# Kernel optimization log

Measured on AMD Instinct MI355X. Metric: run time of the kernel, lower is better.

The kernel has to match this reference:

```python
import jax, jax.numpy as jnp
from jax import lax
import numpy as np

B, S, PRE = 64, 12, 12
N04, N07, N08 = 307, 883, 170
IN_DIM, HID, ENC = 128, 256, 256


def setup_inputs() -> dict:
    key = jax.random.key(0)
    ks = iter(jax.random.split(key, 64))
    nrm = lambda shape, s=1.0: jax.random.normal(next(ks), shape, jnp.float32) * s
    uni = lambda shape: jax.random.uniform(next(ks), shape, jnp.float32)
    d = {
        "vec_pems04": nrm((N04, IN_DIM)),
        "vec_pems07": nrm((N07, IN_DIM)),
        "vec_pems08": nrm((N08, IN_DIM)),
        "feat": nrm((B, S, N04)),
        "adj_pems04": uni((N04, N04)),
        "adj_pems07": uni((N07, N07)),
        "adj_pems08": uni((N08, N08)),
    }
    for p in ("ex4", "ex7", "ex8"):
        d[p + "_W1"] = nrm((IN_DIM, HID), 0.05)
        d[p + "_b1"] = jnp.zeros((HID,), jnp.float32)
        d[p + "_W2"] = nrm((HID, ENC), 0.05)
        d[p + "_b2"] = jnp.zeros((ENC,), jnp.float32)
        d[p + "_g"] = jnp.ones((ENC,), jnp.float32)
        d[p + "_bt"] = jnp.zeros((ENC,), jnp.float32)
        d[p + "_eps"] = jnp.ones((1,), jnp.float32)
    d["gru_W1"] = nrm((HID + 1, 2 * HID), 0.05)
    d["gru_b1"] = jnp.ones((2 * HID,), jnp.float32)  # VGRULinear bias=1.0
    d["gru_W2"] = nrm((HID + 1, HID), 0.05)
    d["gru_b2"] = jnp.zeros((HID,), jnp.float32)
    d["feat_W"] = nrm((ENC, ENC), 0.05)
    d["feat_b"] = jnp.zeros((1,), jnp.float32)
    d["lin_W"] = nrm((HID + ENC, HID), 0.05)
    d["lin_b"] = jnp.zeros((HID,), jnp.float32)
    d["out_W"] = nrm((HID, PRE), 0.05)
    d["out_b"] = jnp.zeros((PRE,), jnp.float32)
    d["eval_flag"] = 0
    return d


def _extract(vec, adj, W1, b1, W2, b2, g, bt, eps1):
    # Extractor_N2V with etype='gin', BatchNorm1d in training mode (batch stats)
    h = vec @ W1 + b1
    pooled = adj @ h
    deg = adj @ jnp.ones((adj.shape[0], 1), adj.dtype)
    h = pooled / deg + eps1 * h
    mu = jnp.mean(h, axis=0)
    var = jnp.mean(jnp.square(h - mu), axis=0)  # biased var, as torch BN
    h = (h - mu) * lax.rsqrt(var + 1e-5) * g + bt
    return h @ W2 + b2


def _predict(feat, node_feat, gru_W1, gru_b1, gru_W2, gru_b2, feat_W, feat_b, lin_W, lin_b):
    Bb, Ss, N = feat.shape
    H = gru_W2.shape[1]
    E = node_feat.shape[-1]
    # feat @ weights + bias is timestep-invariant -> hoist out of the scan (same math)
    fp = jnp.broadcast_to(node_feat[None], (Bb, N, E)).reshape(Bb * N, E) @ feat_W + feat_b

    def vl(x, hs, W, b):
        # VGRULinear: concat scalar input with per-node hidden, flatten per node
        cat = jnp.concatenate([x[..., None], hs.reshape(Bb, N, H)], axis=2).reshape(Bb * N, H + 1)
        return (cat @ W + b).reshape(Bb, -1)

    def step(h, x):
        gates = jax.nn.sigmoid(vl(x, h, gru_W1, gru_b1))  # (B, N*2H)
        r, u = jnp.split(gates, 2, axis=1)                # chunk on flat dim, as in source
        c = jnp.tanh(vl(x, r * h, gru_W2, gru_b2))
        nh = u * h + (1.0 - u) * c
        nh = jnp.concatenate([nh.reshape(Bb * N, H), fp], axis=1) @ lin_W + lin_b
        nh = nh.reshape(Bb, N * H)
        return nh, None

    h0 = jnp.zeros((Bb, N * H), feat.dtype)
    hT, _ = lax.scan(step, h0, jnp.swapaxes(feat, 0, 1))  # scan over seq_len
    return hT.reshape(Bb * N, H)  # last output


def reference(vec_pems04, vec_pems07, vec_pems08, feat, adj_pems04, adj_pems07, adj_pems08,
              ex4_W1, ex4_b1, ex4_W2, ex4_b2, ex4_g, ex4_bt, ex4_eps,
              ex7_W1, ex7_b1, ex7_W2, ex7_b2, ex7_g, ex7_bt, ex7_eps,
              ex8_W1, ex8_b1, ex8_W2, ex8_b2, ex8_g, ex8_bt, ex8_eps,
              gru_W1, gru_b1, gru_W2, gru_b2, feat_W, feat_b, lin_W, lin_b,
              out_W, out_b, eval_flag):
    # dataset='4' != ft_dataset='8', eval=False branch
    f4 = _extract(vec_pems04, adj_pems04, ex4_W1, ex4_b1, ex4_W2, ex4_b2, ex4_g, ex4_bt, ex4_eps)
    f7 = _extract(vec_pems07, adj_pems07, ex7_W1, ex7_b1, ex7_W2, ex7_b2, ex7_g, ex7_bt, ex7_eps)
    f8 = _extract(vec_pems08, adj_pems08, ex8_W1, ex8_b1, ex8_W2, ex8_b2, ex8_g, ex8_bt, ex8_eps)
    last = _predict(feat, f4, gru_W1, gru_b1, gru_W2, gru_b2, feat_W, feat_b, lin_W, lin_b)
    pred = (last @ out_W + out_b).reshape(feat.shape[0], adj_pems04.shape[0], -1)
    return pred, f4, f7, f8
```

## Files before the change

### kernel.cpp

```cpp
#include <hip/hip_runtime.h>
#include <hip/hip_bf16.h>
#include <math.h>

using bf16 = __hip_bfloat16;
using short8  = __attribute__((ext_vector_type(8))) short;
using float4v = __attribute__((ext_vector_type(4))) float;

#define B_   64
#define S_   12
#define N04  307
#define N07  883
#define N08  170
#define BN   (B_ * N04)
#define HID  256
#define ENC  256
#define PRE  12
#define UOFF (N04 * HID)

constexpr int c_Mi[3]   = {N04, N07, N08};
constexpr int c_Kp[3]   = {320, 896, 192};
constexpr int c_Moff[3] = {0, N04, N04 + N07};
constexpr int c_Aoff[3] = {0, N04 * 320, N04 * 320 + N07 * 896};
constexpr int c_Cb[3]   = {0, 320, 320 + 896};
#define MTOT  (N04 + N07 + N08)
#define H0T_LD 1408

#define NT 38
constexpr int g_sz[NT] = {
    39296, 113024, 21760, 235776, 94249, 779689, 28900,
    32768, 256, 65536, 256, 256, 256, 1,
    32768, 256, 65536, 256, 256, 256, 1,
    32768, 256, 65536, 256, 256, 256, 1,
    131584, 512, 65792, 256, 65536, 1, 131072, 256, 3072, 12
};
struct Tables { int off[NT + 1]; int blk[NT + 1]; };
constexpr Tables mk_tables() {
    Tables t{};
    t.off[0] = 0; t.blk[0] = 0;
    for (int i = 0; i < NT; ++i) {
        t.off[i + 1] = t.off[i] + g_sz[i];
        t.blk[i + 1] = t.blk[i] + (g_sz[i] + 1023) / 1024;
    }
    return t;
}
constexpr Tables g_tbl = mk_tables();

static __device__ __forceinline__ float fsigmoid(float t) {
    return __builtin_amdgcn_rcpf(1.f + __expf(-t));
}
static __device__ __forceinline__ float ftanh(float t) {
    return 1.f - 2.f * __builtin_amdgcn_rcpf(__expf(2.f * t) + 1.f);
}

static __device__ __forceinline__ void bsplit(int m, int& b, int& nn) {
    b  = (int)(((unsigned long long)(unsigned)m * 27980243ull) >> 33);
    nn = m - b * N04;
}

__global__ void sniff_kernel(const unsigned short* raw, int* flag)
{
    __shared__ int sh[256];
    int t = threadIdx.x, cnt = 0;
    for (int i = t; i < 2048; i += 256) {
        unsigned int w = ((unsigned int)raw[i]) << 16;
        float a = fabsf(__uint_as_float(w));
        if (a > 1e-3f && a < 100.f) cnt++;
    }
    sh[t] = cnt; __syncthreads();
    for (int off = 128; off > 0; off >>= 1) {
        if (t < off) sh[t] += sh[t + off];
        __syncthreads();
    }
    if (t == 0) *flag = (sh[0] > 1536) ? 1 : 0;
}

struct Ptrs { const void* p[NT]; };

__global__ __launch_bounds__(256) void convert_all(Ptrs a, float* arena, const int* flag)
{
    const int bf = *flag;
    int b = blockIdx.x;
    int t = 0;
    while (b >= g_tbl.blk[t + 1]) ++t;
    const int base = (b - g_tbl.blk[t]) * 1024;
    const int n = g_sz[t];
    const void* src = a.p[t];
    float* dst = arena + g_tbl.off[t];
#pragma unroll
    for (int k = 0; k < 4; ++k) {
        int j = base + k * 256 + threadIdx.x;
        if (j < n)
            dst[j] = bf ? __bfloat162float(((const bf16*)src)[j]) : ((const float*)src)[j];
    }
}

__global__ __launch_bounds__(256) void prep_weights(const float* w1, const float* w2, const float* wl,
                                                    bf16* WgP, bf16* WcP, bf16* WlP)
{
    int id = blockIdx.x * 256 + threadIdx.x;
    if (id < 131072) {
        int tile = id >> 9, within = id & 511;
        int lane = within >> 3, e = within & 7;
        int n = (tile >> 3) * 16 + (lane & 15);
        int k = (tile & 7) * 32 + (lane >> 4) * 8 + e;
        WgP[id] = __float2bfloat16(w1[(size_t)(1 + k) * 512 + n]);
    } else if (id < 196608) {
        int r = id - 131072;
        int tile = r >> 9, within = r & 511;
        int lane = within >> 3, e = within & 7;
        int n = (tile >> 3) * 16 + (lane & 15);
        int k = (tile & 7) * 32 + (lane >> 4) * 8 + e;
        WcP[r] = __float2bfloat16(w2[(size_t)(1 + k) * 256 + n]);
    } else if (id < 262144) {
        int r = id - 196608;
        int tile = r >> 9, within = r & 511;
        int lane = within >> 3, e = within & 7;
        int n = (tile >> 3) * 16 + (lane & 15);
        int k = (tile & 7) * 32 + (lane >> 4) * 8 + e;
        WlP[r] = __float2bfloat16(wl[(size_t)k * 256 + n]);
    }
}

__global__ __launch_bounds__(256) void prep_adjB(const float* a4, const float* a7, const float* a8, bf16* adjB)
{
    int z = blockIdx.z;
    int Mi = c_Mi[z], Kp = c_Kp[z];
    int m = blockIdx.x;
    if (m >= Mi) return;
    const float* src = (z == 0) ? a4 : (z == 1) ? a7 : a8;
    bf16* dst = adjB + c_Aoff[z] + (size_t)m * Kp;
    for (int c = threadIdx.x; c < Kp; c += 256)
        dst[c] = (c < Mi) ? __float2bfloat16(src[(size_t)m * Mi + c]) : __float2bfloat16(0.f);
}

__global__ __launch_bounds__(256) void prep_transposes(
    const float* v4, const float* v7, const float* v8,
    const float* w1a, const float* w1b, const float* w1c,
    const float* w2a, const float* w2b, const float* w2c,
    const float* featW, const float* linW, const float* outW,
    bf16* vecB, bf16* W1T, bf16* W2T, bf16* featWT, bf16* linW2T, bf16* outWP)
{
    int id = blockIdx.x * 256 + threadIdx.x;
    if (id < 174080) {
        int r = id >> 7, c = id & 127;
        float v = (r < N04) ? v4[(size_t)r * 128 + c]
                : (r < N04 + N07) ? v7[(size_t)(r - N04) * 128 + c]
                : v8[(size_t)(r - N04 - N07) * 128 + c];
        vecB[id] = __float2bfloat16(v);
    } else if (id < 174080 + 98304) {
        int r = id - 174080; int z = r >> 15; int rem = r & 32767;
        int n = rem >> 7, k = rem & 127;
        const float* w = (z == 0) ? w1a : (z == 1) ? w1b : w1c;
        W1T[r] = __float2bfloat16(w[(size_t)k * 256 + n]);
    } else if (id < 272384 + 196608) {
        int r = id - 272384; int z = r >> 16; int rem = r & 65535;
        int n = rem >> 8, k = rem & 255;
        const float* w = (z == 0) ? w2a : (z == 1) ? w2b : w2c;
        W2T[r] = __float2bfloat16(w[(size_t)k * 256 + n]);
    } else if (id < 468992 + 65536) {
        int r = id - 468992; int n = r >> 8, k = r & 255;
        featWT[r] = __float2bfloat16(featW[(size_t)k * 256 + n]);
    } else if (id < 534528 + 65536) {
        int r = id - 534528; int n = r >> 8, k = r & 255;
        linW2T[r] = __float2bfloat16(linW[(size_t)(256 + k) * 256 + n]);
    } else if (id < 600064 + 16384) {
        int r = id - 600064;
        int tile = r >> 9, within = r & 511;
        int lane = within >> 3, e = within & 7;
        int p = (tile >> 3) * 16 + (lane & 15);
        int k = (tile & 7) * 32 + (lane >> 4) * 8 + e;
        outWP[r] = __float2bfloat16((p < PRE) ? outW[(size_t)k * PRE + p] : 0.f);
    }
}
#define PREP_T_TOT (600064 + 16384)

struct GemmZ {
    const unsigned short* A[3];
    const unsigned short* BT[3];
    int M[3]; int K[3]; int lda[3]; int ldb[3];
};

template <typename EP>
__global__ __launch_bounds__(256) void gemm_mfma64(GemmZ p, int Nv, EP ep)
{
    const int z = blockIdx.z;
    const int gx = gridDim.x, gy = gridDim.y;
    const int nwg = gx * gy;
    const int flat = blockIdx.y * gx + blockIdx.x;
    const int xcd = flat & 7, lin = flat >> 3;
    const int q = nwg >> 3, r = nwg & 7;
    const int wg = (xcd < r ? xcd * (q + 1) : r * (q + 1) + (xcd - r) * q) + lin;
    const int bx = wg / gy;
    const int by = wg - bx * gy;

    const int M = p.M[z], K = p.K[z], lda = p.lda[z], ldb = p.ldb[z];
    const int m0 = bx * 64;
    const int n0 = by * 64;
    if (m0 >= M) return;
    __shared__ __align__(16) unsigned short As[64 * 72];
    __shared__ __align__(16) unsigned short Bs[64 * 72];
    const int t = threadIdx.x;
    const int srow  = t >> 2;
    const int skoff = (t & 3) * 16;
    const int lane = t & 63;
    const int w  = t >> 6;
    const int wm = (w & 1) * 32;
    const int wn = (w >> 1) * 32;
    const int l15 = lane & 15;
    const int l4  = lane >> 4;

    float4v acc[2][2];
#pragma unroll
    for (int i = 0; i < 2; ++i)
#pragma unroll
        for (int j = 0; j < 2; ++j) acc[i][j] = (float4v)(0.f);

    const int gm = m0 + srow;
    const bool avalid = (gm < M);
    const unsigned short* aptr = p.A[z]  + (size_t)gm * lda + skoff;
    const unsigned short* bptr = p.BT[z] + (size_t)(n0 + srow) * ldb + skoff;
    unsigned short* asw = &As[srow * 72 + skoff];
    unsigned short* bsw = &Bs[srow * 72 + skoff];
    const uint4 z4 = {0, 0, 0, 0};

    for (int kt = 0; kt < K; kt += 64) {
        uint4 av0 = avalid ? *(const uint4*)(aptr + kt)     : z4;
        uint4 av1 = avalid ? *(const uint4*)(aptr + kt + 8) : z4;
        uint4 bv0 = *(const uint4*)(bptr + kt);
        uint4 bv1 = *(const uint4*)(bptr + kt + 8);
        __syncthreads();
        *(uint4*)(asw)     = av0;
        *(uint4*)(asw + 8) = av1;
        *(uint4*)(bsw)     = bv0;
        *(uint4*)(bsw + 8) = bv1;
        __syncthreads();
#pragma unroll
        for (int ks = 0; ks < 2; ++ks) {
            short8 af[2], bq[2];
#pragma unroll
            for (int mi = 0; mi < 2; ++mi)
                af[mi] = *(const short8*)&As[(wm + mi * 16 + l15) * 72 + ks * 32 + l4 * 8];
#pragma unroll
            for (int ni = 0; ni < 2; ++ni)
                bq[ni] = *(const short8*)&Bs[(wn + ni * 16 + l15) * 72 + ks * 32 + l4 * 8];
#pragma unroll
            for (int mi = 0; mi < 2; ++mi)
#pragma unroll
                for (int ni = 0; ni < 2; ++ni)
                    acc[mi][ni] = __builtin_amdgcn_mfma_f32_16x16x32_bf16(af[mi], bq[ni], acc[mi][ni], 0, 0, 0);
        }
    }
#pragma unroll
    for (int mi = 0; mi < 2; ++mi) {
#pragma unroll
        for (int r2 = 0; r2 < 4; ++r2) {
            int m = m0 + wm + mi * 16 + l4 * 4 + r2;
            if (m >= M) continue;
#pragma unroll
            for (int ni = 0; ni < 2; ++ni) {
                int n = n0 + wn + ni * 16 + l15;
                if (n < Nv) ep(z, m, n, acc[mi][ni][r2]);
            }
        }
    }
}

struct GemmB { const unsigned short* A; const unsigned short* Bp; int M; };

template <typename EP>
__global__ __launch_bounds__(256, 4) void gemm_bd(GemmB p, int Nv, EP ep)
{
    const int gx = gridDim.x, gy = gridDim.y;
    const int nwg = gx * gy;
    const int flat = blockIdx.y * gx + blockIdx.x;
    const int xcd = flat & 7, lin = flat >> 3;
    const int q = nwg >> 3, r = nwg & 7;
    const int wg = (xcd < r ? xcd * (q + 1) : r * (q + 1) + (xcd - r) * q) + lin;
    const int bx = wg / gy;
    const int by = wg - bx * gy;
    const int m0 = bx * 64;
    const int n0 = by * 64;

    __shared__ __align__(16) unsigned short As[64 * 72];
    const int t = threadIdx.x;
    const int srow  = t >> 2;
    const int skoff = (t & 3) * 16;
    const int lane = t & 63;
    const int w  = t >> 6;
    const int wm = (w & 1) * 32;
    const int wn = (w >> 1) * 32;
    const int l15 = lane & 15;
    const int l4  = lane >> 4;

    float4v acc[2][2];
#pragma unroll
    for (int i = 0; i < 2; ++i)
#pragma unroll
        for (int j = 0; j < 2; ++j) acc[i][j] = (float4v)(0.f);

    const unsigned short* aptr = p.A + (size_t)(m0 + srow) * 256 + skoff;
    unsigned short* asw = &As[srow * 72 + skoff];
    const unsigned short* bbase = p.Bp + (((size_t)((n0 + wn) >> 4) * 8) << 9) + (lane << 3);

#pragma unroll
    for (int kt = 0; kt < 4; ++kt) {
        uint4 av0 = *(const uint4*)(aptr + kt * 64);
        uint4 av1 = *(const uint4*)(aptr + kt * 64 + 8);
        __syncthreads();
        *(uint4*)(asw)     = av0;
        *(uint4*)(asw + 8) = av1;
        __syncthreads();
#pragma unroll
        for (int ks = 0; ks < 2; ++ks) {
            const int kc = kt * 2 + ks;
            short8 af[2], bq[2];
#pragma unroll
            for (int mi = 0; mi < 2; ++mi)
                af[mi] = *(const short8*)&As[(wm + mi * 16 + l15) * 72 + ks * 32 + l4 * 8];
            bq[0] = *(const short8*)(bbase + ((size_t)kc << 9));
            bq[1] = *(const short8*)(bbase + ((size_t)(kc + 8) << 9));
#pragma unroll
            for (int mi = 0; mi < 2; ++mi)
#pragma unroll
                for (int ni = 0; ni < 2; ++ni)
                    acc[mi][ni] = __builtin_amdgcn_mfma_f32_16x16x32_bf16(af[mi], bq[ni], acc[mi][ni], 0, 0, 0);
        }
    }
#pragma unroll
    for (int mi = 0; mi < 2; ++mi) {
#pragma unroll
        for (int r2 = 0; r2 < 4; ++r2) {
            const int m = m0 + wm + mi * 16 + l4 * 4 + r2;
#pragma unroll
            for (int ni = 0; ni < 2; ++ni) {
                const int n = n0 + wn + ni * 16 + l15;
                if (n < Nv) ep(0, m, n, acc[mi][ni][r2]);
            }
        }
    }
}

struct EPg1 {
    const float* b1[3]; float* h0F; bf16* h0T;
    __device__ void operator()(int z, int m, int n, float v) const {
        v += b1[z][n];
        int gr = c_Moff[z] + m;
        h0F[(size_t)gr * 256 + n] = v;
        h0T[(size_t)n * H0T_LD + c_Cb[z] + m] = __float2bfloat16(v);
    }
};
struct EPg2 {
    const float* deg; const float* h0F; float* h1F; const float* eps[3];
    __device__ void operator()(int z, int m, int n, float v) const {
        int gr = c_Moff[z] + m;
        h1F[(size_t)gr * 256 + n] = v / deg[gr] + eps[z][0] * h0F[(size_t)gr * 256 + n];
    }
};
struct EPg3 {
    const float* b2[3]; void* outbase; size_t ooff[3]; const int* flag; bf16* f4B;
    __device__ void operator()(int z, int m, int n, float v) const {
        v += b2[z][n];
        size_t i = ooff[z] + (size_t)m * 256 + n;
        if (*flag) ((bf16*)outbase)[i] = __float2bfloat16(v);
        else       ((float*)outbase)[i] = v;
        if (z == 0) f4B[(size_t)m * 256 + n] = __float2bfloat16(v);
    }
};
struct EPfp2a {
    const float* sb; bf16* fpreB;
    __device__ void operator()(int z, int m, int n, float v) const {
        fpreB[(size_t)m * 256 + n] = __float2bfloat16(v + sb[0]);
    }
};
struct EPfp2b {
    float* fp2;
    __device__ void operator()(int z, int m, int n, float v) const {
        fp2[(size_t)m * 256 + n] = v;
    }
};
struct EPpred {
    const float* ob; void* outbase; const int* flag;
    __device__ void operator()(int z, int m, int n, float v) const {
        v += ob[n];
        size_t i = (size_t)m * PRE + n;
        if (*flag) ((bf16*)outbase)[i] = __float2bfloat16(v);
        else       ((float*)outbase)[i] = v;
    }
};

struct EPgates3 {
    bf16* rh; bf16* ub; const bf16* hB;
    const float* b1; const float* w1r0; const float* feat; int s;
    __device__ void operator()(int z, int m, int n, float v) const {
        int b, nn; bsplit(m, b, nn);
        float x = feat[((size_t)b * S_ + s) * N04 + nn];
        float g = fsigmoid(v + b1[n] + x * w1r0[n]);
        int p = nn * 512 + n;
        int base = b * UOFF;
        if (p < UOFF) {
            int idx = base + p;
            rh[idx] = __float2bfloat16(g * __bfloat162float(hB[idx]));
        } else {
            ub[base + (p - UOFF)] = __float2bfloat16(g);
        }
    }
};
struct EPcand3 {
    bf16* uhc; const bf16* ub; const bf16* hB;
    const float* b2; const float* w2r0; const float* feat; int s;
    __device__ void operator()(int z, int m, int n, float v) const {
        int b, nn; bsplit(m, b, nn);
        float x = feat[((size_t)b * S_ + s) * N04 + nn];
        float c = ftanh(v + b2[n] + x * w2r0[n]);
        size_t idx = (size_t)m * 256 + n;
        float u = __bfloat162float(ub[idx]);
        float h = __bfloat162float(hB[idx]);
        uhc[idx] = __float2bfloat16(u * h + (1.f - u) * c);
    }
};
struct EPlin3 {
    bf16* hB; const float* lb; const float* fp2;
    __device__ void operator()(int z, int m, int n, float v) const {
        int b, nn; bsplit(m, b, nn);
        hB[(size_t)m * 256 + n] = __float2bfloat16(v + lb[n] + fp2[(size_t)nn * 256 + n]);
    }
};

__global__ __launch_bounds__(256) void init_step0(const float* feat,
                                                  const float* b1, const float* w1r0,
                                                  const float* b2, const float* w2r0,
                                                  bf16* uhc)
{
    int m = blockIdx.x, n = threadIdx.x;
    int b, nn; bsplit(m, b, nn);
    const float* fb = feat + (size_t)b * S_ * N04;
    float c = ftanh(b2[n] + fb[nn] * w2r0[n]);
    int p = UOFF + nn * 256 + n;
    int gn = p >> 9, gc = p & 511;
    float u = fsigmoid(b1[gc] + fb[gn] * w1r0[gc]);
    uhc[(size_t)m * 256 + n] = __float2bfloat16((1.f - u) * c);
}

__global__ void deg_all(const float* a4, const float* a7, const float* a8, float* deg)
{
    int z = blockIdx.z;
    int Mi = c_Mi[z];
    int row = blockIdx.x;
    if (row >= Mi) return;
    const float* adj = (z == 0) ? a4 : (z == 1) ? a7 : a8;
    float s = 0.f;
    for (int j = threadIdx.x; j < Mi; j += 64) s += adj[(size_t)row * Mi + j];
#pragma unroll
    for (int off = 32; off > 0; off >>= 1) s += __shfl_down(s, off, 64);
    if (threadIdx.x == 0) deg[c_Moff[z] + row] = s;
}

__global__ __launch_bounds__(256) void stats_all(const float* h1F, float* mu, float* rstd)
{
    int z = blockIdx.z;
    int Mi = c_Mi[z], moff = c_Moff[z];
    int j = blockIdx.x;
    int t = threadIdx.x;
    float s = 0.f, ss = 0.f;
    for (int i = t; i < Mi; i += 256) {
        float v = h1F[(size_t)(moff + i) * 256 + j];
        s += v; ss += v * v;
    }
    __shared__ float sh[256], sh2[256];
    sh[t] = s; sh2[t] = ss;
    __syncthreads();
    for (int off = 128; off > 0; off >>= 1) {
        if (t < off) { sh[t] += sh[t + off]; sh2[t] += sh2[t + off]; }
        __syncthreads();
    }
    if (t == 0) {
        float m = sh[0] / (float)Mi;
        float var = sh2[0] / (float)Mi - m * m;
        mu[z * 256 + j] = m;
        rstd[z * 256 + j] = rsqrtf(var + 1e-5f);
    }
}

__global__ __launch_bounds__(256) void norm_all(const float* h1F, const float* mu, const float* rstd,
                                                const float* ga, const float* gb, const float* gc,
                                                const float* ba, const float* bb, const float* bc,
                                                bf16* nh1B)
{
    int r = blockIdx.x;
    int n = threadIdx.x;
    int z = (r < N04) ? 0 : (r < N04 + N07) ? 1 : 2;
    const float* g  = (z == 0) ? ga : (z == 1) ? gb : gc;
    const float* bt = (z == 0) ? ba : (z == 1) ? bb : bc;
    float v = (h1F[(size_t)r * 256 + n] - mu[z * 256 + n]) * rstd[z * 256 + n] * g[n] + bt[n];
    nh1B[(size_t)r * 256 + n] = __float2bfloat16(v);
}

extern "C" void kernel_launch(void* const* d_in, const int* in_sizes, int n_in,
                              void* d_out, int out_size, void* d_ws, size_t ws_size,
                              hipStream_t stream)
{
    char* wp = (char*)d_ws;
    auto carve = [&](size_t bytes) -> void* {
        void* p = (void*)wp;
        wp += (bytes + 255) & ~(size_t)255;
        return p;
    };
    float* arena = (float*)carve((size_t)g_tbl.off[NT] * 4);
    int*   flag  = (int*)carve(256);
    bf16*  hb_a  = (bf16*)carve((size_t)BN * HID * 2);
    bf16*  hb_b  = (bf16*)carve((size_t)BN * HID * 2);
    bf16*  rh    = (bf16*)carve((size_t)BN * HID * 2);
    bf16*  uhc   = (bf16*)carve((size_t)BN * HID * 2);
    bf16*  ubufB = (bf16*)carve((size_t)BN * HID * 2);
    bf16*  WgP   = (bf16*)carve((size_t)512 * 256 * 2);
    bf16*  WcP   = (bf16*)carve((size_t)256 * 256 * 2);
    bf16*  WlP   = (bf16*)carve((size_t)256 * 256 * 2);
    bf16*  vecB  = (bf16*)carve((size_t)MTOT * 128 * 2);
    bf16*  adjB  = (bf16*)carve((size_t)(N04 * 320 + N07 * 896 + N08 * 192) * 2);
    bf16*  W1T   = (bf16*)carve((size_t)3 * 256 * 128 * 2);
    bf16*  W2T   = (bf16*)carve((size_t)3 * 256 * 256 * 2);
    bf16*  featWT= (bf16*)carve((size_t)256 * 256 * 2);
    bf16*  linW2T= (bf16*)carve((size_t)256 * 256 * 2);
    bf16*  outWP = (bf16*)carve((size_t)64 * 256 * 2);
    float* h0F   = (float*)carve((size_t)MTOT * 256 * 4);
    bf16*  h0T   = (bf16*)carve((size_t)256 * H0T_LD * 2);
    float* h1F   = (float*)carve((size_t)MTOT * 256 * 4);
    bf16*  nh1B  = (bf16*)carve((size_t)MTOT * 256 * 2);
    float* degb  = (float*)carve((size_t)MTOT * 4);
    float* mub   = (float*)carve(3 * 256 * 4);
    float* rstdb = (float*)carve(3 * 256 * 4);
    bf16*  f4B   = (bf16*)carve((size_t)N04 * 256 * 2);
    bf16*  fpreB = (bf16*)carve((size_t)N04 * 256 * 2);
    float* fp2   = (float*)carve((size_t)N04 * 256 * 4);

    sniff_kernel<<<1, 256, 0, stream>>>((const unsigned short*)d_in[0], flag);
    Ptrs ptrs;
    for (int i = 0; i < NT; ++i) ptrs.p[i] = d_in[i];
    convert_all<<<g_tbl.blk[NT], 256, 0, stream>>>(ptrs, arena, flag);

    auto A = [&](int i) -> const float* { return arena + g_tbl.off[i]; };

    prep_weights<<<1024, 256, 0, stream>>>(A(28), A(30), A(34), WgP, WcP, WlP);
    prep_adjB<<<dim3(N07, 1, 3), 256, 0, stream>>>(A(4), A(5), A(6), adjB);
    prep_transposes<<<(PREP_T_TOT + 255) / 256, 256, 0, stream>>>(
        A(0), A(1), A(2), A(7), A(14), A(21), A(9), A(16), A(23),
        A(32), A(34), A(36), vecB, W1T, W2T, featWT, linW2T, outWP);

    hipMemsetAsync(h0T, 0, (size_t)256 * H0T_LD * 2, stream);

    const size_t o_f4 = (size_t)B_ * N04 * PRE;
    const size_t o_f7 = o_f4 + (size_t)N04 * ENC;
    const size_t o_f8 = o_f7 + (size_t)N07 * ENC;

    deg_all<<<dim3(N07, 1, 3), 64, 0, stream>>>(A(4), A(5), A(6), degb);

    {
        GemmZ p;
        for (int z = 0; z < 3; ++z) {
            p.A[z] = (const unsigned short*)(vecB + (size_t)c_Moff[z] * 128);
            p.BT[z] = (const unsigned short*)(W1T + (size_t)z * 256 * 128);
            p.M[z] = c_Mi[z]; p.K[z] = 128; p.lda[z] = 128; p.ldb[z] = 128;
        }
        EPg1 ep{{A(8), A(15), A(22)}, h0F, h0T};
        gemm_mfma64<<<dim3(14, 4, 3), 256, 0, stream>>>(p, 256, ep);
    }
    {
        GemmZ p;
        for (int z = 0; z < 3; ++z) {
            p.A[z] = (const unsigned short*)(adjB + c_Aoff[z]);
            p.BT[z] = (const unsigned short*)(h0T + c_Cb[z]);
            p.M[z] = c_Mi[z]; p.K[z] = c_Kp[z]; p.lda[z] = c_Kp[z]; p.ldb[z] = H0T_LD;
        }
        EPg2 ep{degb, h0F, h1F, {A(13), A(20), A(27)}};
        gemm_mfma64<<<dim3(14, 4, 3), 256, 0, stream>>>(p, 256, ep);
    }
    stats_all<<<dim3(256, 1, 3), 256, 0, stream>>>(h1F, mub, rstdb);
    norm_all<<<MTOT, 256, 0, stream>>>(h1F, mub, rstdb, A(11), A(18), A(25), A(12), A(19), A(26), nh1B);
    {
        GemmZ p;
        for (int z = 0; z < 3; ++z) {
            p.A[z] = (const unsigned short*)(nh1B + (size_t)c_Moff[z] * 256);
            p.BT[z] = (const unsigned short*)(W2T + (size_t)z * 256 * 256);
            p.M[z] = c_Mi[z]; p.K[z] = 256; p.lda[z] = 256; p.ldb[z] = 256;
        }
        EPg3 ep{{A(10), A(17), A(24)}, d_out, {o_f4, o_f7, o_f8}, flag, f4B};
        gemm_mfma64<<<dim3(14, 4, 3), 256, 0, stream>>>(p, 256, ep);
    }
    {
        GemmZ p{};
        p.A[0] = (const unsigned short*)f4B; p.BT[0] = (const unsigned short*)featWT;
        p.M[0] = N04; p.K[0] = 256; p.lda[0] = 256; p.ldb[0] = 256;
        gemm_mfma64<<<dim3(5, 4, 1), 256, 0, stream>>>(p, 256, EPfp2a{A(33), fpreB});
        p.A[0] = (const unsigned short*)fpreB; p.BT[0] = (const unsigned short*)linW2T;
        gemm_mfma64<<<dim3(5, 4, 1), 256, 0, stream>>>(p, 256, EPfp2b{fp2});
    }

    const float* feat = A(3);
    bf16* hcB = hb_a;
    bf16* hnB = hb_b;
    for (int s = 0; s < S_; ++s) {
        if (s == 0) {
            init_step0<<<BN, 256, 0, stream>>>(feat, A(29), A(28), A(31), A(30), uhc);
        } else {
            GemmB pg{(const unsigned short*)hcB, (const unsigned short*)WgP, BN};
            gemm_bd<<<dim3(BN / 64, 8, 1), 256, 0, stream>>>(pg, 512,
                EPgates3{rh, ubufB, hcB, A(29), A(28), feat, s});
            GemmB pc{(const unsigned short*)rh, (const unsigned short*)WcP, BN};
            gemm_bd<<<dim3(BN / 64, 4, 1), 256, 0, stream>>>(pc, 256,
                EPcand3{uhc, ubufB, hcB, A(31), A(30), feat, s});
        }
        GemmB pl{(const unsigned short*)uhc, (const unsigned short*)WlP, BN};
        gemm_bd<<<dim3(BN / 64, 4, 1), 256, 0, stream>>>(pl, 256,
            EPlin3{hnB, A(35), fp2});
        bf16* tb = hcB; hcB = hnB; hnB = tb;
    }

    {
        GemmB pp{(const unsigned short*)hcB, (const unsigned short*)outWP, BN};
        gemm_bd<<<dim3(BN / 64, 1, 1), 256, 0, stream>>>(pp, PRE, EPpred{A(37), d_out, flag});
    }
}
```

Before: 743.8 us.

## Fuse GRU candidate and output-linear GEMMs into one kernel, fold degree into adj prep

Adds a gru_cl kernel that computes the candidate GEMM and its tanh/update epilogue, stages the resulting hidden state in shared memory, and immediately runs the output-linear GEMM on it. This removes the uhc global round trip and one launch per timestep, and folds the step-0 init into the same kernel. The degree row-sum is also computed inside prep_adjB, so the separate deg_all launch goes away. In exchange, each block now covers the full 256-wide N tile with 64 accumulators per thread and a large shared-memory footprint, which may lower occupancy.

Result: slower. 1.302 ms (+75.1%).

```diff
diff --git a/kernel.cpp b/kernel.cpp
--- a/kernel.cpp
+++ b/kernel.cpp
@@ -121,7 +121,8 @@
     }
 }
 
-__global__ __launch_bounds__(256) void prep_adjB(const float* a4, const float* a7, const float* a8, bf16* adjB)
+__global__ __launch_bounds__(256) void prep_adjB(const float* a4, const float* a7, const float* a8,
+                                                 bf16* adjB, float* deg)
 {
     int z = blockIdx.z;
     int Mi = c_Mi[z], Kp = c_Kp[z];
@@ -129,8 +130,19 @@
     if (m >= Mi) return;
     const float* src = (z == 0) ? a4 : (z == 1) ? a7 : a8;
     bf16* dst = adjB + c_Aoff[z] + (size_t)m * Kp;
-    for (int c = threadIdx.x; c < Kp; c += 256)
-        dst[c] = (c < Mi) ? __float2bfloat16(src[(size_t)m * Mi + c]) : __float2bfloat16(0.f);
+    float s = 0.f;
+    for (int c = threadIdx.x; c < Kp; c += 256) {
+        float v = (c < Mi) ? src[(size_t)m * Mi + c] : 0.f;
+        dst[c] = __float2bfloat16(v);
+        s += v;
+    }
+    __shared__ float sh[256];
+    sh[threadIdx.x] = s; __syncthreads();
+    for (int off = 128; off > 0; off >>= 1) {
+        if (threadIdx.x < off) sh[threadIdx.x] += sh[threadIdx.x + off];
+        __syncthreads();
+    }
+    if (threadIdx.x == 0) deg[c_Moff[z] + m] = sh[0];
 }
 
 __global__ __launch_bounds__(256) void prep_transposes(
@@ -340,6 +352,131 @@
     }
 }
 
+struct GruCL {
+    const unsigned short* rhA; const bf16* ub; const bf16* hB;
+    const unsigned short* WcP; const unsigned short* WlP;
+    const float* b2; const float* w2r0; const float* feat;
+    const float* lb; const float* fp2;
+    const float* b1; const float* w1r0;
+    bf16* hn; int s;
+};
+
+template <int STEP0>
+__global__ __launch_bounds__(256) void gru_cl(GruCL p)
+{
+    __shared__ __align__(16) unsigned short As[64 * 72];
+    __shared__ __align__(16) unsigned short U[64 * 264];
+    const int t = threadIdx.x;
+    const int lane = t & 63, w = t >> 6;
+    const int wm = (w & 1) * 32;
+    const int wn = (w >> 1) * 128;
+    const int l15 = lane & 15, l4 = lane >> 4;
+    const int m0 = blockIdx.x * 64;
+    const int srow = t >> 2, skoff = (t & 3) * 16;
+
+    if (STEP0) {
+        for (int j = t; j < 64 * 256; j += 256) {
+            int r_loc = j >> 8, n = j & 255;
+            int b, nn; bsplit(m0 + r_loc, b, nn);
+            const float* fb = p.feat + (size_t)b * S_ * N04;
+            float c = ftanh(p.b2[n] + fb[nn] * p.w2r0[n]);
+            int pf = UOFF + nn * 256 + n;
+            int gn = pf >> 9, gc = pf & 511;
+            float u = fsigmoid(p.b1[gc] + fb[gn] * p.w1r0[gc]);
+            ((bf16*)U)[r_loc * 264 + n] = __float2bfloat16((1.f - u) * c);
+        }
+    } else {
+        float4v acc[2][8];
+#pragma unroll
+        for (int i = 0; i < 2; ++i)
+#pragma unroll
+            for (int j = 0; j < 8; ++j) acc[i][j] = (float4v)(0.f);
+        const unsigned short* aptr = p.rhA + (size_t)(m0 + srow) * 256 + skoff;
+        unsigned short* asw = &As[srow * 72 + skoff];
+        const unsigned short* bbase = p.WcP + (((size_t)(wn >> 4) * 8) << 9) + (lane << 3);
+#pragma unroll
+        for (int kt = 0; kt < 4; ++kt) {
+            uint4 av0 = *(const uint4*)(aptr + kt * 64);
+            uint4 av1 = *(const uint4*)(aptr + kt * 64 + 8);
+            __syncthreads();
+            *(uint4*)(asw)     = av0;
+            *(uint4*)(asw + 8) = av1;
+            __syncthreads();
+#pragma unroll
+            for (int ks = 0; ks < 2; ++ks) {
+                const int kc = kt * 2 + ks;
+                short8 af[2];
+#pragma unroll
+                for (int mi = 0; mi < 2; ++mi)
+                    af[mi] = *(const short8*)&As[(wm + mi * 16 + l15) * 72 + ks * 32 + l4 * 8];
+#pragma unroll
+                for (int ni = 0; ni < 8; ++ni) {
+                    short8 bq = *(const short8*)(bbase + (((size_t)ni * 8 + kc) << 9));
+                    acc[0][ni] = __builtin_amdgcn_mfma_f32_16x16x32_bf16(af[0], bq, acc[0][ni], 0, 0, 0);
+                    acc[1][ni] = __builtin_amdgcn_mfma_f32_16x16x32_bf16(af[1], bq, acc[1][ni], 0, 0, 0);
+                }
+            }
+        }
+        float xr[2][4];
+#pragma unroll
+        for (int mi = 0; mi < 2; ++mi)
+#pragma unroll
+            for (int r2 = 0; r2 < 4; ++r2) {
+                int b, nn; bsplit(m0 + wm + mi * 16 + l4 * 4 + r2, b, nn);
+                xr[mi][r2] = p.feat[((size_t)b * S_ + p.s) * N04 + nn];
+            }
+#pragma unroll
+        for (int mi = 0; mi < 2; ++mi)
+#pragma unroll
+            for (int r2 = 0; r2 < 4; ++r2) {
+                const int r_loc = wm + mi * 16 + l4 * 4 + r2;
+                const size_t mrow = (size_t)(m0 + r_loc) * 256;
+#pragma unroll
+                for (int ni = 0; ni < 8; ++ni) {
+                    const int n = wn + ni * 16 + l15;
+                    float c = ftanh(acc[mi][ni][r2] + p.b2[n] + xr[mi][r2] * p.w2r0[n]);
+                    float u = __bfloat162float(p.ub[mrow + n]);
+                    float h = __bfloat162float(p.hB[mrow + n]);
+                    ((bf16*)U)[r_loc * 264 + n] = __float2bfloat16(u * h + (1.f - u) * c);
+                }
+            }
+    }
+    __syncthreads();
+
+    float4v acl[2][8];
+#pragma unroll
+    for (int i = 0; i < 2; ++i)
+#pragma unroll
+        for (int j = 0; j < 8; ++j) acl[i][j] = (float4v)(0.f);
+    const unsigned short* lbase = p.WlP + (((size_t)(wn >> 4) * 8) << 9) + (lane << 3);
+#pragma unroll
+    for (int kc = 0; kc < 8; ++kc) {
+        short8 af[2];
+#pragma unroll
+        for (int mi = 0; mi < 2; ++mi)
+            af[mi] = *(const short8*)&U[(wm + mi * 16 + l15) * 264 + kc * 32 + l4 * 8];
+#pragma unroll
+        for (int ni = 0; ni < 8; ++ni) {
+            short8 bq = *(const short8*)(lbase + (((size_t)ni * 8 + kc) << 9));
+            acl[0][ni] = __builtin_amdgcn_mfma_f32_16x16x32_bf16(af[0], bq, acl[0][ni], 0, 0, 0);
+            acl[1][ni] = __builtin_amdgcn_mfma_f32_16x16x32_bf16(af[1], bq, acl[1][ni], 0, 0, 0);
+        }
+    }
+#pragma unroll
+    for (int mi = 0; mi < 2; ++mi)
+#pragma unroll
+        for (int r2 = 0; r2 < 4; ++r2) {
+            const int m = m0 + wm + mi * 16 + l4 * 4 + r2;
+            int b, nn; bsplit(m, b, nn);
+#pragma unroll
+            for (int ni = 0; ni < 8; ++ni) {
+                const int n = wn + ni * 16 + l15;
+                p.hn[(size_t)m * 256 + n] =
+                    __float2bfloat16(acl[mi][ni][r2] + p.lb[n] + p.fp2[(size_t)nn * 256 + n]);
+            }
+        }
+}
+
 struct EPg1 {
     const float* b1[3]; float* h0F; bf16* h0T;
     __device__ void operator()(int z, int m, int n, float v) const {
@@ -405,55 +542,6 @@
         }
     }
 };
-struct EPcand3 {
-    bf16* uhc; const bf16* ub; const bf16* hB;
-    const float* b2; const float* w2r0; const float* feat; int s;
-    __device__ void operator()(int z, int m, int n, float v) const {
-        int b, nn; bsplit(m, b, nn);
-        float x = feat[((size_t)b * S_ + s) * N04 + nn];
-        float c = ftanh(v + b2[n] + x * w2r0[n]);
-        size_t idx = (size_t)m * 256 + n;
-        float u = __bfloat162float(ub[idx]);
-        float h = __bfloat162float(hB[idx]);
-        uhc[idx] = __float2bfloat16(u * h + (1.f - u) * c);
-    }
-};
-struct EPlin3 {
-    bf16* hB; const float* lb; const float* fp2;
-    __device__ void operator()(int z, int m, int n, float v) const {
-        int b, nn; bsplit(m, b, nn);
-        hB[(size_t)m * 256 + n] = __float2bfloat16(v + lb[n] + fp2[(size_t)nn * 256 + n]);
-    }
-};
-
-__global__ __launch_bounds__(256) void init_step0(const float* feat,
-                                                  const float* b1, const float* w1r0,
-                                                  const float* b2, const float* w2r0,
-                                                  bf16* uhc)
-{
-    int m = blockIdx.x, n = threadIdx.x;
-    int b, nn; bsplit(m, b, nn);
-    const float* fb = feat + (size_t)b * S_ * N04;
-    float c = ftanh(b2[n] + fb[nn] * w2r0[n]);
-    int p = UOFF + nn * 256 + n;
-    int gn = p >> 9, gc = p & 511;
-    float u = fsigmoid(b1[gc] + fb[gn] * w1r0[gc]);
-    uhc[(size_t)m * 256 + n] = __float2bfloat16((1.f - u) * c);
-}
-
-__global__ void deg_all(const float* a4, const float* a7, const float* a8, float* deg)
-{
-    int z = blockIdx.z;
-    int Mi = c_Mi[z];
-    int row = blockIdx.x;
-    if (row >= Mi) return;
-    const float* adj = (z == 0) ? a4 : (z == 1) ? a7 : a8;
-    float s = 0.f;
-    for (int j = threadIdx.x; j < Mi; j += 64) s += adj[(size_t)row * Mi + j];
-#pragma unroll
-    for (int off = 32; off > 0; off >>= 1) s += __shfl_down(s, off, 64);
-    if (threadIdx.x == 0) deg[c_Moff[z] + row] = s;
-}
 
 __global__ __launch_bounds__(256) void stats_all(const float* h1F, float* mu, float* rstd)
 {
@@ -510,7 +598,6 @@
     bf16*  hb_a  = (bf16*)carve((size_t)BN * HID * 2);
     bf16*  hb_b  = (bf16*)carve((size_t)BN * HID * 2);
     bf16*  rh    = (bf16*)carve((size_t)BN * HID * 2);
-    bf16*  uhc   = (bf16*)carve((size_t)BN * HID * 2);
     bf16*  ubufB = (bf16*)carve((size_t)BN * HID * 2);
     bf16*  WgP   = (bf16*)carve((size_t)512 * 256 * 2);
     bf16*  WcP   = (bf16*)carve((size_t)256 * 256 * 2);
@@ -541,7 +628,7 @@
     auto A = [&](int i) -> const float* { return arena + g_tbl.off[i]; };
 
     prep_weights<<<1024, 256, 0, stream>>>(A(28), A(30), A(34), WgP, WcP, WlP);
-    prep_adjB<<<dim3(N07, 1, 3), 256, 0, stream>>>(A(4), A(5), A(6), adjB);
+    prep_adjB<<<dim3(N07, 1, 3), 256, 0, stream>>>(A(4), A(5), A(6), adjB, degb);
     prep_transposes<<<(PREP_T_TOT + 255) / 256, 256, 0, stream>>>(
         A(0), A(1), A(2), A(7), A(14), A(21), A(9), A(16), A(23),
         A(32), A(34), A(36), vecB, W1T, W2T, featWT, linW2T, outWP);
@@ -551,8 +638,6 @@
     const size_t o_f4 = (size_t)B_ * N04 * PRE;
     const size_t o_f7 = o_f4 + (size_t)N04 * ENC;
     const size_t o_f8 = o_f7 + (size_t)N07 * ENC;
-
-    deg_all<<<dim3(N07, 1, 3), 64, 0, stream>>>(A(4), A(5), A(6), degb);
 
     {
         GemmZ p;
@@ -599,19 +684,21 @@
     bf16* hcB = hb_a;
     bf16* hnB = hb_b;
     for (int s = 0; s < S_; ++s) {
+        GruCL pc;
+        pc.rhA = (const unsigned short*)rh; pc.ub = ubufB; pc.hB = hcB;
+        pc.WcP = (const unsigned short*)WcP; pc.WlP = (const unsigned short*)WlP;
+        pc.b2 = A(31); pc.w2r0 = A(30); pc.feat = feat;
+        pc.lb = A(35); pc.fp2 = fp2;
+        pc.b1 = A(29); pc.w1r0 = A(28);
+        pc.hn = hnB; pc.s = s;
         if (s == 0) {
-            init_step0<<<BN, 256, 0, stream>>>(feat, A(29), A(28), A(31), A(30), uhc);
+            gru_cl<1><<<BN / 64, 256, 0, stream>>>(pc);
         } else {
             GemmB pg{(const unsigned short*)hcB, (const unsigned short*)WgP, BN};
             gemm_bd<<<dim3(BN / 64, 8, 1), 256, 0, stream>>>(pg, 512,
                 EPgates3{rh, ubufB, hcB, A(29), A(28), feat, s});
-            GemmB pc{(const unsigned short*)rh, (const unsigned short*)WcP, BN};
-            gemm_bd<<<dim3(BN / 64, 4, 1), 256, 0, stream>>>(pc, 256,
-                EPcand3{uhc, ubufB, hcB, A(31), A(30), feat, s});
-        }
-        GemmB pl{(const unsigned short*)uhc, (const unsigned short*)WlP, BN};
-        gemm_bd<<<dim3(BN / 64, 4, 1), 256, 0, stream>>>(pl, 256,
-            EPlin3{hnB, A(35), fp2});
+            gru_cl<0><<<BN / 64, 256, 0, stream>>>(pc);
+        }
         bf16* tb = hcB; hcB = hnB; hnB = tb;
     }
 
```
